# Performance work log

Hardware: AMD Instinct MI355X
Metric: run time of the kernel (lower is better)

The kernel has to match this reference:

```python
import jax, jax.numpy as jnp
import numpy as np

C = 32           # in_channels
KH, KW = 3, 3    # kernel_range
SHIFT = 1
NP = KH * KW


def conv2d(x, w, b, pad):
    # x: NCHW, w: OIHW
    y = jax.lax.conv_general_dilated(
        x, w, window_strides=(1, 1), padding=[(pad, pad), (pad, pad)],
        dimension_numbers=('NCHW', 'OIHW', 'NCHW'))
    return y + b[None, :, None, None]


def setup_inputs() -> dict:
    key = jax.random.key(0)
    ks = jax.random.split(key, 14)
    p = lambda k, shape: (jax.random.normal(k, shape, dtype=jnp.float32) * 0.02)
    inp = {
        'x':  jax.random.normal(ks[0], (4, C, 256, 256), dtype=jnp.float32),
        'wk': p(ks[1], (C * NP, C, 1, 1)), 'bk': p(ks[2], (C * NP,)),
        'wv': p(ks[3], (C * NP, C, 1, 1)), 'bv': p(ks[4], (C * NP,)),
        'wq': p(ks[5], (C, C, 1, 1)),      'bq': p(ks[6], (C,)),
        'w1': p(ks[7], (C, C, 3, 3)),      'b1': p(ks[8], (C,)),
        'w2': p(ks[9], (2 * C, C, 3, 3)),  'b2': p(ks[10], (2 * C,)),
        'w3': p(ks[11], (C, 2 * C, 3, 3)), 'b3': p(ks[12], (C,)),
    }
    return inp


def reference(x, wk, bk, wv, bv, wq, bq, w1, b1, w2, b2, w3, b3):
    B, D, H, W = x.shape
    h_half, w_half = KH // 2, KW // 2
    ph, pw = h_half * SHIFT, w_half * SHIFT

    x_k = conv2d(x, wk, bk, 0)  # (B, D*NP, H, W)
    x_v = conv2d(x, wv, bv, 0)
    x_q = conv2d(x, wq, bq, 0)  # (B, D, H, W)

    pad4 = ((0, 0), (0, 0), (ph, ph), (pw, pw))
    x_k = jnp.pad(x_k, pad4)
    x_v = jnp.pad(x_v, pad4)
    mask_pad = jnp.pad(jnp.ones((B, 1, H, W), x.dtype), pad4)

    k_ls, v_ls, m_ls = [], [], []
    layer = 0
    for i in range(-h_half, h_half + 1):
        for j in range(-w_half, w_half + 1):
            r0 = ph + i * SHIFT
            c0 = pw + j * SHIFT
            k_ls.append(x_k[:, layer * D:(layer + 1) * D, r0:r0 + H, c0:c0 + W])
            v_ls.append(x_v[:, layer * D:(layer + 1) * D, r0:r0 + H, c0:c0 + W])
            m_ls.append(mask_pad[:, :, r0:r0 + H, c0:c0 + W])
            layer += 1

    # Faithful to torch .view semantics: flat row-major reshape, NOT a permute.
    k = jnp.stack(k_ls, axis=1).reshape(B * H * W, NP, D)   # (B,NP,D,H,W) -> flat
    v = jnp.stack(v_ls, axis=1).reshape(B * H * W, NP, D)
    m = jnp.stack(m_ls, axis=1).reshape(B * H * W, NP, 1)
    q = x_q.reshape(B * H * W, 1, D)                         # (B,D,H,W) -> flat

    scores = jnp.matmul(k, jnp.swapaxes(q, -1, -2)) * m / 8.0  # (N, NP, 1)
    alpha = jax.nn.softmax(scores, axis=1)
    res = jnp.matmul(jnp.swapaxes(alpha, -1, -2), v)           # (N, 1, D)
    t = res.reshape(B, D, H, W)

    t = jax.nn.relu(conv2d(t, w1, b1, 1))
    t = jax.nn.relu(conv2d(t, w2, b2, 1))
    t = jax.nn.relu(conv2d(t, w3, b3, 1))
    return t
```

## Files before the change

kernel.cpp:

```cpp
#include <hip/hip_runtime.h>
#include <hip/hip_bf16.h>

#define B_ 4
#define C_ 32
#define H_ 256
#define W_ 256
#define S_ 65536
#define NP_ 9
#define OC_ 288
#define PR 258
#define PWN 264
#define XGUARD 260
#define XSTRIDE 66056

using bf16 = __hip_bfloat16;
typedef __attribute__((ext_vector_type(8)))  short  short8;
typedef __attribute__((ext_vector_type(4)))  short  short4_t;
typedef __attribute__((ext_vector_type(2)))  short  short2_t;
typedef __attribute__((ext_vector_type(16))) float  f32x16;

__device__ __forceinline__ float b2f(short s) {
    return __uint_as_float(((unsigned)(unsigned short)s) << 16);
}

template<int IC, int OC>
__device__ __forceinline__ void prepA_body(int fid, const float* __restrict__ w,
                                           bf16* __restrict__ apk)
{
    constexpr int NK = 9 * IC / 16;
    int tile = fid >> 9;
    int l = (fid >> 3) & 63;
    int j = fid & 7;
    int mt = tile / NK;
    int ks = tile - mt * NK;
    int q = l >> 5;
    int oc = mt * 32 + (l & 31);
    int k = ks * 16 + q * 8 + j;
    int tap = k / IC;
    int ic = k - tap * IC;
    apk[fid] = __float2bfloat16(w[((oc * IC + ic) * 3 + tap / 3) * 3 + tap % 3]);
}

template<int G>
__device__ __forceinline__ void zerob_body(int b, int p, uint4* __restrict__ buf)
{
    int gran;
    if (p < 2 * PWN * G) {
        int row = (p < PWN * G) ? 0 : 257;
        int rem = p % (PWN * G);
        gran = row * PWN * G + rem;
    } else {
        int p2 = p - 2 * PWN * G;
        int col = (p2 < 256 * G) ? 0 : 257;
        int rem = p2 % (256 * G);
        int r = rem / G + 1;
        int icg = rem - (rem / G) * G;
        gran = (r * PWN + col) * G + icg;
    }
    buf[(size_t)b * PR * PWN * G + gran] = uint4{0, 0, 0, 0};
}

__device__ __forceinline__ void prep_body(
    int idx,
    const float* __restrict__ wk, const float* __restrict__ wv,
    const float* __restrict__ wq,
    const float* __restrict__ w1, const float* __restrict__ w2,
    const float* __restrict__ w3,
    bf16* __restrict__ apk0, bf16* __restrict__ apk1,
    bf16* __restrict__ apk2, bf16* __restrict__ apk3,
    uint4* __restrict__ tA, uint4* __restrict__ t1, uint4* __restrict__ t2,
    uint4* __restrict__ xb16)
{
    if (idx < 19456) {
        int j    = idx & 7;
        int lane = (idx >> 3) & 63;
        int ks   = (idx >> 9) & 1;
        int mt   = idx >> 10;
        int oc = lane & 31;
        int ic = ks * 16 + (lane >> 5) * 8 + j;
        const float* w; int ocg;
        if (mt < 9)       { w = wk; ocg = mt * 32 + oc; }
        else if (mt < 18) { w = wv; ocg = (mt - 9) * 32 + oc; }
        else              { w = wq; ocg = oc; }
        apk0[idx] = __float2bfloat16(w[ocg * C_ + ic]);
    } else if (idx < 28672) {
        prepA_body<32, 32>(idx - 19456, w1, apk1);
    } else if (idx < 47104) {
        prepA_body<32, 64>(idx - 28672, w2, apk2);
    } else if (idx < 65536) {
        prepA_body<64, 32>(idx - 47104, w3, apk3);
    } else if (idx < 82176) {
        int i5 = idx - 65536;
        zerob_body<4>(i5 / 4160, i5 % 4160, tA);
    } else if (idx < 98816) {
        int i6 = idx - 82176;
        zerob_body<4>(i6 / 4160, i6 % 4160, t1);
    } else if (idx < 132096) {
        int i7 = idx - 98816;
        zerob_body<8>(i7 / 8320, i7 % 8320, t2);
    } else if (idx < 142464) {
        int i8 = idx - 132096;
        size_t off;
        if (i8 < 8320) {
            int b = i8 / 2080, r = i8 - b * 2080;
            if (r < 1040) off = (size_t)b * (XSTRIDE * 4) + r;
            else          off = ((size_t)b * XSTRIDE + XGUARD + 65536) * 4 + (r - 1040);
        } else {
            off = (size_t)(4 * XSTRIDE) * 4 + (i8 - 8320);
        }
        xb16[off] = uint4{0, 0, 0, 0};
    }
}

__global__ __launch_bounds__(256) void k_qp(
    const float* __restrict__ x,
    const float* __restrict__ wk, const float* __restrict__ wv,
    const float* __restrict__ wq, const float* __restrict__ bq,
    const float* __restrict__ w1, const float* __restrict__ w2,
    const float* __restrict__ w3,
    bf16* __restrict__ apk0, bf16* __restrict__ apk1,
    bf16* __restrict__ apk2, bf16* __restrict__ apk3,
    uint4* __restrict__ tA, uint4* __restrict__ t1, uint4* __restrict__ t2,
    bf16* __restrict__ xqs, bf16* __restrict__ xb16)
{
    __shared__ bf16 lbuf[32][140];
    int tid = threadIdx.x;

    if (blockIdx.x >= 2048) {
        prep_body((blockIdx.x - 2048) * 256 + tid, wk, wv, wq, w1, w2, w3,
                  apk0, apk1, apk2, apk3, tA, t1, t2, (uint4*)xb16);
        return;
    }

    int bh  = blockIdx.x >> 9;
    int blk = blockIdx.x & 511;
    int pixw0 = blk << 7;
    int wvi  = tid >> 6;
    int lane = tid & 63;
    int col  = lane & 31, q = lane >> 5;
    int pix  = pixw0 + wvi * 32 + col;

    const float* xb = x + (size_t)bh * (C_ * S_);

    short8 bfrag[2];
#pragma unroll
    for (int kk = 0; kk < 2; ++kk)
#pragma unroll
        for (int j = 0; j < 8; ++j) {
            bf16 h = __float2bfloat16(xb[(size_t)(kk * 16 + q * 8 + j) * S_ + pix]);
            bfrag[kk][j] = *reinterpret_cast<short*>(&h);
        }

    {
        bf16* xr = xb16 + ((size_t)bh * XSTRIDE + XGUARD + pix) * 32;
        *reinterpret_cast<short8*>(xr + (q << 3))       = bfrag[0];
        *reinterpret_cast<short8*>(xr + ((2 + q) << 3)) = bfrag[1];
    }

    short8 wfrag[2];
#pragma unroll
    for (int kk = 0; kk < 2; ++kk)
#pragma unroll
        for (int j = 0; j < 8; ++j) {
            bf16 h = __float2bfloat16(wq[col * C_ + kk * 16 + q * 8 + j]);
            wfrag[kk][j] = *reinterpret_cast<short*>(&h);
        }

    f32x16 acc = {};
    acc = __builtin_amdgcn_mfma_f32_32x32x16_bf16(bfrag[0], wfrag[0], acc, 0, 0, 0);
    acc = __builtin_amdgcn_mfma_f32_32x32x16_bf16(bfrag[1], wfrag[1], acc, 0, 0, 0);
    float bbv = bq[col];
#pragma unroll
    for (int g4 = 0; g4 < 4; ++g4) {
        short4_t sv;
#pragma unroll
        for (int j = 0; j < 4; ++j) {
            bf16 hb = __float2bfloat16(acc[g4 * 4 + j] + bbv);
            sv[j] = *reinterpret_cast<short*>(&hb);
        }
        *reinterpret_cast<short4_t*>(&lbuf[col][wvi * 32 + 8 * g4 + 4 * q]) = sv;
    }
    __syncthreads();
    int ch0 = tid >> 4, chk = tid & 15, ch1 = ch0 + 16;
    short8 v0 = *reinterpret_cast<const short8*>(&lbuf[ch0][chk * 8]);
    short8 v1 = *reinterpret_cast<const short8*>(&lbuf[ch1][chk * 8]);
    int tb = (pixw0 >> 5) + (chk >> 2);
    int G2 = chk & 3;
    bf16* qb = xqs + (size_t)bh * (32 * S_);
    short4_t lo0 = {v0[0], v0[1], v0[2], v0[3]}, hi0 = {v0[4], v0[5], v0[6], v0[7]};
    short4_t lo1 = {v1[0], v1[1], v1[2], v1[3]}, hi1 = {v1[4], v1[5], v1[6], v1[7]};
    *reinterpret_cast<short4_t*>(qb + (ch0 * 2048 + tb) * 32 + G2 * 4)      = lo0;
    *reinterpret_cast<short4_t*>(qb + (ch0 * 2048 + tb) * 32 + 16 + G2 * 4) = hi0;
    *reinterpret_cast<short4_t*>(qb + (ch1 * 2048 + tb) * 32 + G2 * 4)      = lo1;
    *reinterpret_cast<short4_t*>(qb + (ch1 * 2048 + tb) * 32 + 16 + G2 * 4) = hi1;
}


#define Q_LOAD(T, PN, QA, QB)                                                         \
{                                                                                     \
    int Tg = tgbase + (T);                                                            \
    if (Tg < 2048) {                                                                  \
        int plane_base_n = (((PN) << 5) + col) << 16;                                 \
        unsigned n = (unsigned)plane_base_n + ((unsigned)Tg << 5);                    \
        unsigned tl = n / 288u;                                                       \
        const bf16* qp = xqb + ((size_t)tl << 5) + (q << 4);                          \
        QA = *reinterpret_cast<const short8*>(qp);                                    \
        QB = *reinterpret_cast<const short8*>(qp + 8);                                \
    }                                                                                 \
}

#define DO_TILE(T, SQ, QAv, QBv)                                                      \
{                                                                                     \
    int Tg = tgbase + (T);                                                            \
    if (Tg < 2048) {                                                                  \
        short8 qA = QAv;                                                              \
        short8 qB = QBv;                                                              \
        int xib = ((T) << 5) + 257 + shf + col;                                       \
        int swx = (xib ^ (xib >> 2)) & 3;                                             \
        short8 fa = *reinterpret_cast<const short8*>(&xs[xib * 4 + (q ^ swx)]);       \
        short8 fb = *reinterpret_cast<const short8*>(&xs[xib * 4 + ((2 + q) ^ swx)]); \
        bool hbad  = ((((T) << 5) < hb_lo) || (((T) << 5) >= hb_hi));                 \
        bool tb_lo = (dj == -1) && ((Tg & 7) == 0);                                   \
        bool tb_hi = (dj == 1) && ((Tg & 7) == 7);                                    \
        if (tb_lo && q == 0) qA[0] = 0;                                               \
        if (tb_hi && q == 1) qB[7] = 0;                                               \
        f32x16 ka = {bK, bK, bK, bK, bK, bK, bK, bK, bK, bK, bK, bK, bK, bK, bK, bK}; \
        ka = __builtin_amdgcn_mfma_f32_32x32x16_bf16(fa, apkv[(p * 2 + 0) * 64 + lane], ka, 0, 0, 0); \
        ka = __builtin_amdgcn_mfma_f32_32x32x16_bf16(fb, apkv[(p * 2 + 1) * 64 + lane], ka, 0, 0, 0); \
        float dot = 0.f;                                                              \
        _Pragma("unroll")                                                             \
        for (int j3 = 0; j3 < 4; ++j3) {                                              \
            dot += ka[j3]      * b2f(qA[j3]);                                         \
            dot += ka[4 + j3]  * b2f(qA[4 + j3]);                                     \
            dot += ka[8 + j3]  * b2f(qB[j3]);                                         \
            dot += ka[12 + j3] * b2f(qB[4 + j3]);                                     \
        }                                                                             \
        if (hbad) dot = 0.f;                                                          \
        dot += __shfl_xor(dot, 32);                                                   \
        if (q == (SQ)) scL[(T) * 32 + col] = dot;                                     \
        f32x16 vh = {bV, bV, bV, bV, bV, bV, bV, bV, bV, bV, bV, bV, bV, bV, bV, bV}; \
        vh = __builtin_amdgcn_mfma_f32_32x32x16_bf16(fa, apkv[((9 + p) * 2 + 0) * 64 + lane], vh, 0, 0, 0); \
        vh = __builtin_amdgcn_mfma_f32_32x32x16_bf16(fb, apkv[((9 + p) * 2 + 1) * 64 + lane], vh, 0, 0, 0); \
        _Pragma("unroll")                                                             \
        for (int G2 = 0; G2 < 4; ++G2) {                                              \
            short4_t sv;                                                              \
            _Pragma("unroll")                                                         \
            for (int j3 = 0; j3 < 4; ++j3) {                                          \
                float val = hbad ? 0.f : vh[G2 * 4 + j3];                             \
                bf16 hcv = __float2bfloat16(val);                                     \
                sv[j3] = *reinterpret_cast<short*>(&hcv);                             \
            }                                                                         \
            if (G2 == 0 && tb_lo && q == 0) sv[0] = 0;                                \
            if (G2 == 3 && tb_hi && q == 1) sv[3] = 0;                                \
            *reinterpret_cast<short4_t*>(kvB + col * 1616 +                           \
                ((((T) << 2) + (G2 ^ xcol)) << 4) + q * 8) = sv;                      \
        }                                                                             \
    }                                                                                 \
}

__global__ __launch_bounds__(1024, 4) void k_fused(
    const bf16* __restrict__ xb16,
    const bf16* __restrict__ apk,
    const float* __restrict__ bk, const float* __restrict__ bv,
    const bf16* __restrict__ xqs,
    bf16* __restrict__ att)
{
    extern __shared__ char smem_raw[];
    uint4* xs  = reinterpret_cast<uint4*>(smem_raw);
    char*  kvB = smem_raw + 84096;
    float* scL = reinterpret_cast<float*>(smem_raw + 135808);
    unsigned short* scM = reinterpret_cast<unsigned short*>(smem_raw + 139008);

    int bb = blockIdx.x >> 7;
    int s0 = (blockIdx.x & 127) << 9;
    int tgbase = s0 >> 5;

    int tid  = threadIdx.x;
    int lane = tid & 63;
    int wv   = tid >> 6;
    int col  = lane & 31;
    int q    = lane >> 5;
    int xcol = (col >> 3) & 3;

    size_t qbase = ((size_t)bb << 21);
    const bf16* xqb = xqs + qbase;
    const short8* apkv = reinterpret_cast<const short8*>(apk);

    {
        const uint4* src = reinterpret_cast<const uint4*>(xb16) +
                           ((size_t)bb * XSTRIDE + XGUARD + s0 - 257) * 4;
        for (int i = tid; i < 5256; i += 1024) {
            int xi = i >> 2, g = i & 3;
            int sw = (xi ^ (xi >> 2)) & 3;
            xs[xi * 4 + (g ^ sw)] = src[i];
        }
    }

    if (tid < 576) {
        int krow = tid >= 288;
        int i2 = tid - (krow ? 288 : 0);
        int pp = i2 >> 5, dpc = i2 & 31;
        int plane_base_r = ((pp << 5) + dpc) << 16;
        unsigned tl = ((unsigned)(plane_base_r + s0 + 287)) / 288u + (unsigned)krow;
        int sk0 = (int)(tl * 288u) - plane_base_r;
        unsigned m = 0;
        if (sk0 < s0 + 512 && sk0 <= 65248) {
            m = 0x8000u;
#pragma unroll
            for (int seg = 0; seg < 9; ++seg) {
                int rm = (int)tl * 9 + seg;
                int pm = rm >> 16, sm = rm & 65535;
                int dim = pm / 3 - 1, djm = pm - (pm / 3) * 3 - 1;
                int hm = sm >> 8, wm = sm & 255;
                bool mval = ((unsigned)(hm + dim) < 256u) && ((unsigned)(wm + djm) < 256u);
                m |= (mval ? 1u : 0u) << seg;
            }
        }
        scM[tid] = (unsigned short)m;
    }

    short8 qA0, qB0, qA1, qB1;
    Q_LOAD(wv, 0, qA0, qB0)
    if (wv < 9) { Q_LOAD(wv + 16, 0, qA1, qB1) }

    __syncthreads();

    int grp  = tid >> 3, sub = tid & 7;
    int dp   = grp & 31;
    int krow = (grp >> 5) & 1;
    int hh   = sub >> 1;
    int sh   = sub & 1;
    bool athr = tid < 512;
    int swz = (dp >> 3) & 3;

#pragma unroll 1
    for (int p = 0; p < 9; ++p) {
        int di = p / 3 - 1, dj = p - (p / 3) * 3 - 1;
        int shf = di * 256 + dj;
        int hb_lo = (di == -1) ? (256 - s0) : (-0x40000000);
        int hb_hi = (di == 1) ? (65280 - s0) : 0x40000000;
        float bK = bk[p * 32 + col];
        float bV = bv[p * 32 + col];

        DO_TILE(wv, 0, qA0, qB0)
        if (wv < 9) { DO_TILE(wv + 16, 1, qA1, qB1) }

        if (p < 8) {
            Q_LOAD(wv, p + 1, qA0, qB0)
            if (wv < 9) { Q_LOAD(wv + 16, p + 1, qA1, qB1) }
        }
        __syncthreads();

        if (athr) {
            unsigned mflags = scM[krow * 288 + p * 32 + dp];
            if (mflags & 0x8000u) {
                int plane_base_r = ((p << 5) + dp) << 16;
                unsigned tl = ((unsigned)(plane_base_r + s0 + 287)) / 288u + (unsigned)krow;
                int sk0 = (int)(tl * 288u) - plane_base_r;
                int t0 = (sk0 - s0) >> 5;
                float sc[9];
#pragma unroll
                for (int seg = 0; seg < 9; ++seg)
                    sc[seg] = ((mflags >> seg) & 1u) ? scL[(t0 + seg) * 32 + dp] * 0.125f : 0.f;
                float mx = sc[0];
#pragma unroll
                for (int s2 = 1; s2 < 9; ++s2) mx = fmaxf(mx, sc[s2]);
                float wgt[9];
                float sum = 0.f;
#pragma unroll
                for (int s2 = 0; s2 < 9; ++s2) { wgt[s2] = __expf(sc[s2] - mx); sum += wgt[s2]; }
                float inv_ = 1.f / sum;

                float oacc[4] = {0.f, 0.f, 0.f, 0.f};
#pragma unroll
                for (int seg = 0; seg < 9; ++seg) {
                    short4_t vg = *reinterpret_cast<const short4_t*>(
                        kvB + dp * 1616 + ((((t0 + seg) << 2) + (hh ^ swz)) << 4) + sh * 8);
                    float w_ = wgt[seg];
#pragma unroll
                    for (int j = 0; j < 4; ++j) oacc[j] += w_ * b2f(vg[j]);
                }
                short4_t sv;
#pragma unroll
                for (int j = 0; j < 4; ++j) {
                    bf16 h = __float2bfloat16(oacc[j] * inv_);
                    sv[j] = *reinterpret_cast<short*>(&h);
                }
                *reinterpret_cast<short4_t*>(att + qbase + ((size_t)tl << 5) + hh * 8 + sh * 4) = sv;
            }
        }
        __syncthreads();
    }
}

__global__ __launch_bounds__(320) void k_strad(
    const bf16* __restrict__ xb16,
    const float* __restrict__ wk, const float* __restrict__ bk,
    const float* __restrict__ wv, const float* __restrict__ bv,
    const bf16* __restrict__ xqs, bf16* __restrict__ att)
{
    __shared__ float kL[288], vL[288], qL[32], wgtL[10];
    int e = blockIdx.x;
    int b = e >> 8, i = e & 255;
    int g = i >> 3, u = i & 7;
    int tl = g * 2048 + (((2040 + u) * 1593) & 2047);
    int tid = threadIdx.x;

    if (tid < 288) {
        int f  = tl * 288 + tid;
        int cp = f >> 16;
        int sp = f & 65535;
        int tap = cp >> 5;
        int di = tap / 3 - 1, dj = tap - (tap / 3) * 3 - 1;
        int h = sp >> 8, w = sp & 255;
        bool valid = ((unsigned)(h + di) < 256u) && ((unsigned)(w + dj) < 256u);
        float kv_ = 0.f, vv_ = 0.f;
        if (valid) {
            int sx = sp + di * 256 + dj;
            const bf16* xp = xb16 + ((size_t)b * XSTRIDE + XGUARD + sx) * 32;
            const float* wkp = wk + cp * 32;
            const float* wvp = wv + cp * 32;
            float ks = bk[cp], vs = bv[cp];
            short8 xg[4];
#pragma unroll
            for (int gg = 0; gg < 4; ++gg)
                xg[gg] = *reinterpret_cast<const short8*>(xp + gg * 8);
#pragma unroll
            for (int gg = 0; gg < 4; ++gg)
#pragma unroll
                for (int j = 0; j < 8; ++j) {
                    float xv_ = b2f(xg[gg][j]);
                    ks += wkp[gg * 8 + j] * xv_;
                    vs += wvp[gg * 8 + j] * xv_;
                }
            kv_ = ks; vv_ = vs;
        }
        kL[tid] = kv_; vL[tid] = vv_;
    }
    if (tid < 32) {
        int pos = ((tid >> 2) & 1) * 16 + (tid >> 3) * 4 + (tid & 3);
        bf16 hv = xqs[(size_t)b * (32 * S_) + (size_t)tl * 32 + pos];
        qL[tid] = b2f(*reinterpret_cast<short*>(&hv));
    }
    __syncthreads();
    if (tid < 9) {
        float dot = 0.f;
#pragma unroll
        for (int d = 0; d < 32; ++d) dot += kL[tid * 32 + d] * qL[d];
        int rm = tl * 9 + tid;
        int pm = rm >> 16, sm = rm & 65535;
        int dim = pm / 3 - 1, djm = pm - (pm / 3) * 3 - 1;
        int hm = sm >> 8, wm = sm & 255;
        bool mval = ((unsigned)(hm + dim) < 256u) && ((unsigned)(wm + djm) < 256u);
        wgtL[tid] = mval ? dot * 0.125f : 0.f;
    }
    __syncthreads();
    if (tid == 0) {
        float mx = wgtL[0];
#pragma unroll
        for (int s2 = 1; s2 < 9; ++s2) mx = fmaxf(mx, wgtL[s2]);
        float sum = 0.f;
#pragma unroll
        for (int s2 = 0; s2 < 9; ++s2) { wgtL[s2] = __expf(wgtL[s2] - mx); sum += wgtL[s2]; }
        wgtL[9] = 1.f / sum;
    }
    __syncthreads();
    if (tid < 32) {
        float acc = 0.f;
#pragma unroll
        for (int seg = 0; seg < 9; ++seg) acc += wgtL[seg] * vL[seg * 32 + tid];
        att[(size_t)b * 2097152 + (size_t)tl * 32 + tid] = __float2bfloat16(acc * wgtL[9]);
    }
}

__global__ __launch_bounds__(256) void k_repack(
    const bf16* __restrict__ att, bf16* __restrict__ tA)
{
    int idx = blockIdx.x * 256 + threadIdx.x;
    int icg = idx & 3;
    int ps  = idx >> 2;
    int b = ps >> 16;
    int s = ps & 65535;
    const bf16* src = att + (size_t)b * (32 * S_) + icg * 8 * S_ + s;
    short8 v;
#pragma unroll
    for (int j = 0; j < 8; ++j)
        v[j] = *reinterpret_cast<const short*>(src + (size_t)j * S_);
    int row = (s >> 8) + 1, colp = (s & 255) + 1;
    *reinterpret_cast<short8*>(tA + ((size_t)((b * PR + row) * PWN + colp)) * 32 + icg * 8) = v;
}

template<int IC, int OC, bool NCHW_OUT>
__global__ __launch_bounds__(256) void k_conv3s(
    const bf16* __restrict__ in,
    const bf16* __restrict__ apk,
    const float* __restrict__ bs,
    void* __restrict__ outv)
{
    constexpr int G    = IC / 8;
    constexpr int M    = OC / 32;
    constexpr int KPT  = IC / 16;
    constexpr int NK   = 9 * KPT;
    constexpr int NT   = 2;
    constexpr int ROWP = 66;
    constexpr int ROWG = ROWP * G;
    constexpr int TOTG = 6 * ROWG;

    __shared__ uint4 smem[TOTG];

    int wg   = blockIdx.x;
    int orig = (wg & 7) * 128 + (wg >> 3);
    int b   = orig >> 8;
    int rem = orig & 255;
    int h0  = (rem >> 2) << 2;
    int w0  = (rem & 3) * 64;

    int tid = threadIdx.x;

    {
        const uint4* src = reinterpret_cast<const uint4*>(in);
#pragma unroll
        for (int i = 0; i < (TOTG + 255) / 256; ++i) {
            int idx = tid + i * 256;
            if (idx < TOTG) {
                int dr = idx / ROWG;
                int r2 = idx - dr * ROWG;
                uint4 v = src[((size_t)(b * PR + h0 + dr) * PWN + w0) * G + r2];
                int px = r2 >> ((G == 4) ? 2 : 3);
                int sw = (G == 4) ? ((px ^ (px >> 2)) & 3) : (px & 7);
                smem[dr * ROWG + (r2 & ~(G - 1)) + ((r2 ^ sw) & (G - 1))] = v;
            }
        }
    }
    __syncthreads();

    int lane = tid & 63;
    int wid  = tid >> 6;
    int col  = lane & 31, q = lane >> 5;
    int h    = h0 + wid;

    const short8* apkv = reinterpret_cast<const short8*>(apk);

    f32x16 acc[NT][M];
#pragma unroll
    for (int nt = 0; nt < NT; ++nt)
#pragma unroll
        for (int mt = 0; mt < M; ++mt) acc[nt][mt] = (f32x16){};

#pragma unroll
    for (int tap = 0; tap < 9; ++tap) {
        int dr = tap / 3 + wid;
        int dj = tap % 3;
#pragma unroll
        for (int icq = 0; icq < KPT; ++icq) {
            short8 bfr[NT];
#pragma unroll
            for (int nt = 0; nt < NT; ++nt) {
                int px = nt * 32 + col + dj;
                int sw = (G == 4) ? ((px ^ (px >> 2)) & 3) : (px & 7);
                bfr[nt] = *reinterpret_cast<const short8*>(
                    &smem[dr * ROWG + px * G + ((icq * 2 + q) ^ sw)]);
            }
#pragma unroll
            for (int mt = 0; mt < M; ++mt) {
                short8 afr = apkv[(mt * NK + tap * KPT + icq) * 64 + lane];
#pragma unroll
                for (int nt = 0; nt < NT; ++nt)
                    acc[nt][mt] = __builtin_amdgcn_mfma_f32_32x32x16_bf16(
                        afr, bfr[nt], acc[nt][mt], 0, 0, 0);
            }
        }
    }

#pragma unroll
    for (int nt = 0; nt < NT; ++nt) {
        int wout = w0 + nt * 32 + col;
#pragma unroll
        for (int mt = 0; mt < M; ++mt) {
            if (NCHW_OUT) {
                float* out = (float*)outv;
#pragma unroll
                for (int r = 0; r < 16; ++r) {
                    int oc = mt * 32 + (r & 3) + 8 * (r >> 2) + 4 * q;
                    out[(size_t)((b * OC + oc) * H_ + h) * W_ + wout] =
                        fmaxf(acc[nt][mt][r] + bs[oc], 0.f);
                }
            } else {
                bf16* out = (bf16*)outv;
                size_t base = (size_t)((b * PR + h + 1) * PWN + wout + 1) * OC + mt * 32 + 4 * q;
#pragma unroll
                for (int g4 = 0; g4 < 4; ++g4) {
                    short4_t sv;
#pragma unroll
                    for (int r4 = 0; r4 < 4; ++r4) {
                        int oc = mt * 32 + 8 * g4 + 4 * q + r4;
                        bf16 hh = __float2bfloat16(fmaxf(acc[nt][mt][g4 * 4 + r4] + bs[oc], 0.f));
                        sv[r4] = *reinterpret_cast<short*>(&hh);
                    }
                    *reinterpret_cast<short4_t*>(out + base + 8 * g4) = sv;
                }
            }
        }
    }
}

extern "C" void kernel_launch(void* const* d_in, const int* in_sizes, int n_in,
                              void* d_out, int out_size, void* d_ws, size_t ws_size,
                              hipStream_t stream)
{
    const float* x  = (const float*)d_in[0];
    const float* wk = (const float*)d_in[1];
    const float* bk = (const float*)d_in[2];
    const float* wv = (const float*)d_in[3];
    const float* bv = (const float*)d_in[4];
    const float* wq = (const float*)d_in[5];
    const float* bq = (const float*)d_in[6];
    const float* w1 = (const float*)d_in[7];
    const float* b1 = (const float*)d_in[8];
    const float* w2 = (const float*)d_in[9];
    const float* b2 = (const float*)d_in[10];
    const float* w3 = (const float*)d_in[11];
    const float* b3 = (const float*)d_in[12];
    float* out = (float*)d_out;
    char* ws = (char*)d_ws;

    bf16* xqs  = (bf16*)(ws);
    bf16* tA   = (bf16*)(ws + 16777216);
    bf16* t1   = (bf16*)(ws + 34213888);
    bf16* t2   = (bf16*)(ws + 51650560);
    bf16* apk0 = (bf16*)(ws + 86523904);
    bf16* apk1 = (bf16*)(ws + 86562816);
    bf16* apk2 = (bf16*)(ws + 86581248);
    bf16* apk3 = (bf16*)(ws + 86618112);
    bf16* xb16 = (bf16*)(ws + 86654976);
    bf16* attB = (bf16*)d_out;

    static bool attr_set = false;
    if (!attr_set) {
        hipFuncSetAttribute(reinterpret_cast<const void*>(k_fused),
                            hipFuncAttributeMaxDynamicSharedMemorySize, 140160);
        attr_set = true;
    }

    k_qp<<<2605, 256, 0, stream>>>(x, wk, wv, wq, bq, w1, w2, w3,
                                   apk0, apk1, apk2, apk3,
                                   (uint4*)tA, (uint4*)t1, (uint4*)t2,
                                   xqs, xb16);

    k_fused<<<512, 1024, 140160, stream>>>(xb16, apk0, bk, bv, xqs, attB);

    k_strad<<<1024, 320, 0, stream>>>(xb16, wk, bk, wv, bv, xqs, attB);

    k_repack<<<4096, 256, 0, stream>>>(attB, tA);

    k_conv3s<32, 32, false><<<1024, 256, 0, stream>>>(tA, apk1, b1, (void*)t1);
    k_conv3s<32, 64, false><<<1024, 256, 0, stream>>>(t1, apk2, b2, (void*)t2);
    k_conv3s<64, 32, true ><<<1024, 256, 0, stream>>>(t2, apk3, b3, (void*)out);
}
```

Measured before the change: 159.3 us.

## Double-buffer K/V tiles in fused attention and read x directly from global

Drops the shared-memory staging of the x slab and instead loads each tile's input fragments straight from global memory. The k/v and score buffers are double-buffered, so the MFMA projection for position p+1 is computed in the same phase as the softmax/accumulate for position p. This halves the number of barriers per loop iteration and trims shared memory use. The cost is repeated global/L2 loads of x (nine shifted reads per tile) in place of LDS reads.

Measured after the change: 153.3 us, median of 2. 3.7% less time.

```diff
diff --git a/kernel.cpp b/kernel.cpp
--- a/kernel.cpp
+++ b/kernel.cpp
@@ -209,24 +209,23 @@
     }                                                                                 \
 }
 
-#define DO_TILE(T, SQ, QAv, QBv)                                                      \
+#define DO_TILE(T, SQ, QAv, QBv, PP)                                                  \
 {                                                                                     \
     int Tg = tgbase + (T);                                                            \
     if (Tg < 2048) {                                                                  \
         short8 qA = QAv;                                                              \
         short8 qB = QBv;                                                              \
-        int xib = ((T) << 5) + 257 + shf + col;                                       \
-        int swx = (xib ^ (xib >> 2)) & 3;                                             \
-        short8 fa = *reinterpret_cast<const short8*>(&xs[xib * 4 + (q ^ swx)]);       \
-        short8 fb = *reinterpret_cast<const short8*>(&xs[xib * 4 + ((2 + q) ^ swx)]); \
+        const bf16* xp = xbb + (size_t)(XGUARD + (Tg << 5) + shf + col) * 32;         \
+        short8 fa = *reinterpret_cast<const short8*>(xp + (q << 3));                  \
+        short8 fb = *reinterpret_cast<const short8*>(xp + ((2 + q) << 3));            \
         bool hbad  = ((((T) << 5) < hb_lo) || (((T) << 5) >= hb_hi));                 \
         bool tb_lo = (dj == -1) && ((Tg & 7) == 0);                                   \
         bool tb_hi = (dj == 1) && ((Tg & 7) == 7);                                    \
         if (tb_lo && q == 0) qA[0] = 0;                                               \
         if (tb_hi && q == 1) qB[7] = 0;                                               \
         f32x16 ka = {bK, bK, bK, bK, bK, bK, bK, bK, bK, bK, bK, bK, bK, bK, bK, bK}; \
-        ka = __builtin_amdgcn_mfma_f32_32x32x16_bf16(fa, apkv[(p * 2 + 0) * 64 + lane], ka, 0, 0, 0); \
-        ka = __builtin_amdgcn_mfma_f32_32x32x16_bf16(fb, apkv[(p * 2 + 1) * 64 + lane], ka, 0, 0, 0); \
+        ka = __builtin_amdgcn_mfma_f32_32x32x16_bf16(fa, apkv[((PP) * 2 + 0) * 64 + lane], ka, 0, 0, 0); \
+        ka = __builtin_amdgcn_mfma_f32_32x32x16_bf16(fb, apkv[((PP) * 2 + 1) * 64 + lane], ka, 0, 0, 0); \
         float dot = 0.f;                                                              \
         _Pragma("unroll")                                                             \
         for (int j3 = 0; j3 < 4; ++j3) {                                              \
@@ -237,10 +236,10 @@
         }                                                                             \
         if (hbad) dot = 0.f;                                                          \
         dot += __shfl_xor(dot, 32);                                                   \
-        if (q == (SQ)) scL[(T) * 32 + col] = dot;                                     \
+        if (q == (SQ)) scW[(T) * 32 + col] = dot;                                     \
         f32x16 vh = {bV, bV, bV, bV, bV, bV, bV, bV, bV, bV, bV, bV, bV, bV, bV, bV}; \
-        vh = __builtin_amdgcn_mfma_f32_32x32x16_bf16(fa, apkv[((9 + p) * 2 + 0) * 64 + lane], vh, 0, 0, 0); \
-        vh = __builtin_amdgcn_mfma_f32_32x32x16_bf16(fb, apkv[((9 + p) * 2 + 1) * 64 + lane], vh, 0, 0, 0); \
+        vh = __builtin_amdgcn_mfma_f32_32x32x16_bf16(fa, apkv[((9 + (PP)) * 2 + 0) * 64 + lane], vh, 0, 0, 0); \
+        vh = __builtin_amdgcn_mfma_f32_32x32x16_bf16(fb, apkv[((9 + (PP)) * 2 + 1) * 64 + lane], vh, 0, 0, 0); \
         _Pragma("unroll")                                                             \
         for (int G2 = 0; G2 < 4; ++G2) {                                              \
             short4_t sv;                                                              \
@@ -252,11 +251,19 @@
             }                                                                         \
             if (G2 == 0 && tb_lo && q == 0) sv[0] = 0;                                \
             if (G2 == 3 && tb_hi && q == 1) sv[3] = 0;                                \
-            *reinterpret_cast<short4_t*>(kvB + col * 1616 +                           \
+            *reinterpret_cast<short4_t*>(kvW + col * 1616 +                           \
                 ((((T) << 2) + (G2 ^ xcol)) << 4) + q * 8) = sv;                      \
         }                                                                             \
     }                                                                                 \
 }
+
+#define P1_SETUP(PP)                                                                  \
+    int di = (PP) / 3 - 1, dj = (PP) - ((PP) / 3) * 3 - 1;                            \
+    int shf = di * 256 + dj;                                                          \
+    int hb_lo = (di == -1) ? (256 - s0) : (-0x40000000);                              \
+    int hb_hi = (di == 1) ? (65280 - s0) : 0x40000000;                                \
+    float bK = bk[(PP) * 32 + col];                                                   \
+    float bV = bv[(PP) * 32 + col];
 
 __global__ __launch_bounds__(1024, 4) void k_fused(
     const bf16* __restrict__ xb16,
@@ -266,10 +273,11 @@
     bf16* __restrict__ att)
 {
     extern __shared__ char smem_raw[];
-    uint4* xs  = reinterpret_cast<uint4*>(smem_raw);
-    char*  kvB = smem_raw + 84096;
-    float* scL = reinterpret_cast<float*>(smem_raw + 135808);
-    unsigned short* scM = reinterpret_cast<unsigned short*>(smem_raw + 139008);
+    char*  kvB0 = smem_raw;
+    char*  kvB1 = smem_raw + 51712;
+    float* scL0 = reinterpret_cast<float*>(smem_raw + 103424);
+    float* scL1 = reinterpret_cast<float*>(smem_raw + 106624);
+    unsigned short* scM = reinterpret_cast<unsigned short*>(smem_raw + 109824);
 
     int bb = blockIdx.x >> 7;
     int s0 = (blockIdx.x & 127) << 9;
@@ -284,17 +292,8 @@
 
     size_t qbase = ((size_t)bb << 21);
     const bf16* xqb = xqs + qbase;
+    const bf16* xbb = xb16 + (size_t)bb * XSTRIDE * 32;
     const short8* apkv = reinterpret_cast<const short8*>(apk);
-
-    {
-        const uint4* src = reinterpret_cast<const uint4*>(xb16) +
-                           ((size_t)bb * XSTRIDE + XGUARD + s0 - 257) * 4;
-        for (int i = tid; i < 5256; i += 1024) {
-            int xi = i >> 2, g = i & 3;
-            int sw = (xi ^ (xi >> 2)) & 3;
-            xs[xi * 4 + (g ^ sw)] = src[i];
-        }
-    }
 
     if (tid < 576) {
         int krow = tid >= 288;
@@ -322,7 +321,15 @@
     short8 qA0, qB0, qA1, qB1;
     Q_LOAD(wv, 0, qA0, qB0)
     if (wv < 9) { Q_LOAD(wv + 16, 0, qA1, qB1) }
-
+    {
+        P1_SETUP(0)
+        char*  kvW = kvB0;
+        float* scW = scL0;
+        DO_TILE(wv, 0, qA0, qB0, 0)
+        if (wv < 9) { DO_TILE(wv + 16, 1, qA1, qB1, 0) }
+        Q_LOAD(wv, 1, qA0, qB0)
+        if (wv < 9) { Q_LOAD(wv + 16, 1, qA1, qB1) }
+    }
     __syncthreads();
 
     int grp  = tid >> 3, sub = tid & 7;
@@ -335,21 +342,8 @@
 
 #pragma unroll 1
     for (int p = 0; p < 9; ++p) {
-        int di = p / 3 - 1, dj = p - (p / 3) * 3 - 1;
-        int shf = di * 256 + dj;
-        int hb_lo = (di == -1) ? (256 - s0) : (-0x40000000);
-        int hb_hi = (di == 1) ? (65280 - s0) : 0x40000000;
-        float bK = bk[p * 32 + col];
-        float bV = bv[p * 32 + col];
-
-        DO_TILE(wv, 0, qA0, qB0)
-        if (wv < 9) { DO_TILE(wv + 16, 1, qA1, qB1) }
-
-        if (p < 8) {
-            Q_LOAD(wv, p + 1, qA0, qB0)
-            if (wv < 9) { Q_LOAD(wv + 16, p + 1, qA1, qB1) }
-        }
-        __syncthreads();
+        const char*  kvR = (p & 1) ? kvB1 : kvB0;
+        const float* scR = (p & 1) ? scL1 : scL0;
 
         if (athr) {
             unsigned mflags = scM[krow * 288 + p * 32 + dp];
@@ -361,7 +355,7 @@
                 float sc[9];
 #pragma unroll
                 for (int seg = 0; seg < 9; ++seg)
-                    sc[seg] = ((mflags >> seg) & 1u) ? scL[(t0 + seg) * 32 + dp] * 0.125f : 0.f;
+                    sc[seg] = ((mflags >> seg) & 1u) ? scR[(t0 + seg) * 32 + dp] * 0.125f : 0.f;
                 float mx = sc[0];
 #pragma unroll
                 for (int s2 = 1; s2 < 9; ++s2) mx = fmaxf(mx, sc[s2]);
@@ -375,7 +369,7 @@
 #pragma unroll
                 for (int seg = 0; seg < 9; ++seg) {
                     short4_t vg = *reinterpret_cast<const short4_t*>(
-                        kvB + dp * 1616 + ((((t0 + seg) << 2) + (hh ^ swz)) << 4) + sh * 8);
+                        kvR + dp * 1616 + ((((t0 + seg) << 2) + (hh ^ swz)) << 4) + sh * 8);
                     float w_ = wgt[seg];
 #pragma unroll
                     for (int j = 0; j < 4; ++j) oacc[j] += w_ * b2f(vg[j]);
@@ -387,6 +381,18 @@
                     sv[j] = *reinterpret_cast<short*>(&h);
                 }
                 *reinterpret_cast<short4_t*>(att + qbase + ((size_t)tl << 5) + hh * 8 + sh * 4) = sv;
+            }
+        }
+
+        if (p < 8) {
+            P1_SETUP(p + 1)
+            char*  kvW = ((p + 1) & 1) ? kvB1 : kvB0;
+            float* scW = ((p + 1) & 1) ? scL1 : scL0;
+            DO_TILE(wv, 0, qA0, qB0, p + 1)
+            if (wv < 9) { DO_TILE(wv + 16, 1, qA1, qB1, p + 1) }
+            if (p < 7) {
+                Q_LOAD(wv, p + 2, qA0, qB0)
+                if (wv < 9) { Q_LOAD(wv + 16, p + 2, qA1, qB1) }
             }
         }
         __syncthreads();
@@ -638,7 +644,7 @@
     static bool attr_set = false;
     if (!attr_set) {
         hipFuncSetAttribute(reinterpret_cast<const void*>(k_fused),
-                            hipFuncAttributeMaxDynamicSharedMemorySize, 140160);
+                            hipFuncAttributeMaxDynamicSharedMemorySize, 110976);
         attr_set = true;
     }
 
@@ -647,7 +653,7 @@
                                    (uint4*)tA, (uint4*)t1, (uint4*)t2,
                                    xqs, xb16);
 
-    k_fused<<<512, 1024, 140160, stream>>>(xb16, apk0, bk, bv, xqs, attB);
+    k_fused<<<512, 1024, 110976, stream>>>(xb16, apk0, bk, bv, xqs, attB);
 
     k_strad<<<1024, 320, 0, stream>>>(xb16, wk, bk, wv, bv, xqs, attB);
 
```
